# Optimization experiments

Hardware: AMD Instinct MI355X
Metric: run time of the kernel (lower is better)

Reference implementation:

```python
import jax, jax.numpy as jnp
import numpy as np

N_NODES = 100000
N_EDGES = 3200000
D_IN = 256
D_HID = 97


def setup_inputs() -> dict:
    key = jax.random.key(0)
    k1, k2, k3, k4, k5, k6 = jax.random.split(key, 6)
    x = jax.random.normal(k1, (N_NODES, D_IN), dtype=jnp.float32)
    edge_index = jax.random.randint(k2, (2, N_EDGES), 0, N_NODES, dtype=jnp.int64)
    # GCNConv weights (stored as [in, out]) and biases
    W1 = jax.random.normal(k3, (D_IN, D_HID), dtype=jnp.float32) / np.sqrt(D_IN)
    b1 = jnp.zeros((D_HID,), dtype=jnp.float32)
    W2 = jax.random.normal(k4, (D_HID, D_HID), dtype=jnp.float32) / np.sqrt(D_HID)
    b2 = jnp.zeros((D_HID,), dtype=jnp.float32)
    return {"x": x, "edge_index": edge_index, "W1": W1, "b1": b1, "W2": W2, "b2": b2}


def reference(x, edge_index, W1, b1, W2, b2):
    # PyG GCNConv: add self-loops, symmetric degree normalization,
    # out[i] = sum_j norm_ij * (x[j] @ W) + b
    N = x.shape[0]
    self_idx = jnp.arange(N, dtype=edge_index.dtype)
    src = jnp.concatenate([edge_index[0], self_idx])  # source j
    dst = jnp.concatenate([edge_index[1], self_idx])  # target i
    deg = jax.ops.segment_sum(jnp.ones_like(dst, dtype=x.dtype), dst, num_segments=N)
    dinv = jnp.where(deg > 0, 1.0 / jnp.sqrt(deg), 0.0)
    norm = dinv[src] * dinv[dst]  # [E+N]

    def gcn(h, W, b):
        h = h @ W  # dense linear transform first (out_dim small)
        msg = h[src] * norm[:, None]  # gather + scale
        agg = jax.ops.segment_sum(msg, dst, num_segments=N)  # scatter-add
        return agg + b

    h = jax.nn.relu(gcn(x, W1, b1))
    out = gcn(h, W2, b2)
    return out
```

## Files before the change

kernel.cpp:

```cpp
#include <hip/hip_runtime.h>
#include <hip/hip_fp16.h>
#include <stdint.h>

#define D_IN 256
#define D_H  97
#define RST  96
#define NPB  512
#define NBMAX 256
#define CHUNK 4096

typedef _Float16 f16;
typedef f16   f16x8 __attribute__((ext_vector_type(8)));
typedef float f32x4 __attribute__((ext_vector_type(4)));

__device__ __forceinline__ int load_idx(const void* p, int is64, long long pos) {
  if (is64) return (int)(((const long long*)p)[pos]);
  return ((const int*)p)[pos];
}

__global__ void detect_kernel(const void* ei, long long E, int* flag,
                              int* __restrict__ bcur, int nbuck) {
  const int* p32 = (const int*)ei;
  long long stride = E / 1024; if (stride < 1) stride = 1;
  int tid = threadIdx.x;
  for (int i = tid; i <= nbuck; i += 256) bcur[i] = 0;
  int bad = 0;
  for (int s = 0; s < 4; ++s) {
    long long k = ((long long)tid * 4 + s) * stride;
    if (k < E) {
      if (p32[2 * k + 1] != 0) bad = 1;
    }
  }
  __shared__ int sh_bad;
  if (tid == 0) sh_bad = 0;
  __syncthreads();
  if (bad) atomicOr(&sh_bad, 1);
  __syncthreads();
  if (tid == 0) *flag = sh_bad ? 0 : 1;
}

__global__ __launch_bounds__(256) void bucket_scatter_direct(
    const void* ei, const int* __restrict__ flag, int* __restrict__ bcur,
    unsigned int* __restrict__ bsd, long long E, int nbuck, int cap) {
  __shared__ unsigned int packs[CHUNK];
  __shared__ unsigned char bkts[CHUNK];
  __shared__ int hist[NBMAX];
  __shared__ int gpos[NBMAX];
  __shared__ int cur[NBMAX];
  int tid = threadIdx.x;
  if (tid < NBMAX) { hist[tid] = 0; cur[tid] = 0; }
  __syncthreads();
  int f = *flag;
  long long base = (long long)blockIdx.x * CHUNK;
  int cnt = (int)((E - base < CHUNK) ? (E - base) : CHUNK);
  #pragma unroll 4
  for (int i = tid; i < cnt; i += 256) {
    long long e = base + i;
    int s = load_idx(ei, f, e);
    int d = load_idx(ei, f, E + e);
    int b = d >> 9;
    packs[i] = ((unsigned int)(d & (NPB - 1)) << 17) | (unsigned int)s;
    bkts[i] = (unsigned char)b;
    atomicAdd(&hist[b], 1);
  }
  __syncthreads();
  if (tid < nbuck) { int h = hist[tid]; if (h) gpos[tid] = atomicAdd(&bcur[tid], h); }
  __syncthreads();
  #pragma unroll 4
  for (int i = tid; i < cnt; i += 256) {
    int b = bkts[i];
    int r = atomicAdd(&cur[b], 1);
    int idx = gpos[b] + r;
    if (idx < cap) bsd[(size_t)b * cap + idx] = packs[i];
  }
}

__global__ __launch_bounds__(256) void bucket_finalize(
    const unsigned int* __restrict__ bsd, const int* __restrict__ bcur,
    int* __restrict__ row_start, float* __restrict__ dinv,
    int* __restrict__ csr_src, int N, int cap, int nbuck) {
  __shared__ int sc[256];
  __shared__ int h[NPB];
  __shared__ int rs[NPB];
  __shared__ int cur[NPB];
  __shared__ int wsum[4];
  int b = blockIdx.x, tid = threadIdx.x;
  int lane = tid & 63, wid = tid >> 6;
  int v = (tid < nbuck) ? min(bcur[tid], cap) : 0;
  sc[tid] = v;
  h[2 * tid] = 0; h[2 * tid + 1] = 0;
  cur[2 * tid] = 0; cur[2 * tid + 1] = 0;
  __syncthreads();
  for (int o = 1; o < 256; o <<= 1) {
    int a = (tid >= o) ? sc[tid - o] : 0;
    __syncthreads();
    sc[tid] += a;
    __syncthreads();
  }
  int cnt = min(bcur[b], cap);
  int base = sc[b] - cnt;
  if (b == 0 && tid == 0) row_start[N] = sc[255];
  int d0 = b * cap;
  for (int i = tid; i < cnt; i += 256) atomicAdd(&h[bsd[d0 + i] >> 17], 1);
  __syncthreads();
  int a0 = h[2 * tid], a1 = h[2 * tid + 1];
  int tsum = a0 + a1;
  int incl = tsum;
  #pragma unroll
  for (int off = 1; off < 64; off <<= 1) {
    int n = __shfl_up(incl, off, 64);
    if (lane >= off) incl += n;
  }
  if (lane == 63) wsum[wid] = incl;
  __syncthreads();
  int woff = 0;
  for (int k = 0; k < wid; ++k) woff += wsum[k];
  int excl = woff + incl - tsum + base;
  rs[2 * tid] = excl;
  rs[2 * tid + 1] = excl + a0;
  int node0 = b * NPB;
  int n0 = node0 + 2 * tid, n1 = node0 + 2 * tid + 1;
  if (n0 < N) { row_start[n0] = excl;      dinv[n0] = rsqrtf((float)(a0 + 1)); }
  if (n1 < N) { row_start[n1] = excl + a0; dinv[n1] = rsqrtf((float)(a1 + 1)); }
  __syncthreads();
  for (int i = tid; i < cnt; i += 256) {
    unsigned int p = bsd[d0 + i];
    int r = p >> 17;
    int s = (int)(p & 0x1FFFFu);
    int rel = atomicAdd(&cur[r], 1);
    csr_src[rs[r] + rel] = s;
  }
}

__global__ void prep_kernel(const float* __restrict__ W1, const float* __restrict__ b1,
                            const float* __restrict__ W2, const float* __restrict__ b2,
                            f16* __restrict__ W1lin, f16* __restrict__ W2lin,
                            float* __restrict__ b1p, float* __restrict__ b2p) {
  int idx = blockIdx.x * blockDim.x + threadIdx.x;
  const int n1 = 8 * 7 * 512;
  const int n2 = 4 * 7 * 512;
  if (idx < n1) {
    int fid = idx >> 3, hh = idx & 7;
    int lane = fid & 63, fg = fid >> 6;
    int kb = fg / 7, cg = fg % 7;
    int c = cg * 16 + (lane & 15);
    int k = kb * 32 + (lane >> 4) * 8 + hh;
    W1lin[idx] = (f16)((c < D_H && k < 256) ? W1[k * D_H + c] : 0.f);
  } else if (idx < n1 + n2) {
    int j = idx - n1;
    int fid = j >> 3, hh = j & 7;
    int lane = fid & 63, fg = fid >> 6;
    int kb = fg / 7, cg = fg % 7;
    int c = cg * 16 + (lane & 15);
    int k = kb * 32 + (lane >> 4) * 8 + hh;
    W2lin[j] = (f16)((c < D_H && k < D_H) ? W2[k * D_H + c] : 0.f);
  } else if (idx < n1 + n2 + 128) {
    int c = idx - (n1 + n2);
    b1p[c] = (c < D_H) ? b1[c] : 0.0f;
  } else if (idx < n1 + n2 + 256) {
    int c = idx - (n1 + n2 + 128);
    b2p[c] = (c < D_H) ? b2[c] : 0.0f;
  }
}

template<int KI, bool IN_HALF>
__global__ __launch_bounds__(256) void mfma_gemm(
    const float* __restrict__ Af, const f16* __restrict__ Ah,
    const __half2* __restrict__ sideA,
    const f16* __restrict__ Wlin, const float* __restrict__ dinv,
    f16* __restrict__ C, __half2* __restrict__ sideC, int N) {
  int tid = threadIdx.x, wave = tid >> 6, lane = tid & 63;
  int row0 = blockIdx.x * 128;
  int m = lane & 15, q = lane >> 4;
  int kf = q * 8;
  int r0 = row0 + wave * 32 + m;
  int r1 = r0 + 16;
  int rr0 = (r0 < N) ? r0 : 0;
  int rr1 = (r1 < N) ? r1 : 0;
  const f16* wbase = Wlin + lane * 8;

  f16x8 a0[KI], a1[KI];
  #pragma unroll
  for (int kb = 0; kb < KI; ++kb) {
    if constexpr (!IN_HALF) {
      const float* p0 = &Af[(size_t)rr0 * 256 + kb * 32 + kf];
      const float* p1 = &Af[(size_t)rr1 * 256 + kb * 32 + kf];
      float4 u0 = *(const float4*)p0, u1 = *(const float4*)(p0 + 4);
      float4 w0 = *(const float4*)p1, w1 = *(const float4*)(p1 + 4);
      f16x8 t0, t1;
      t0[0] = (f16)u0.x; t0[1] = (f16)u0.y; t0[2] = (f16)u0.z; t0[3] = (f16)u0.w;
      t0[4] = (f16)u1.x; t0[5] = (f16)u1.y; t0[6] = (f16)u1.z; t0[7] = (f16)u1.w;
      t1[0] = (f16)w0.x; t1[1] = (f16)w0.y; t1[2] = (f16)w0.z; t1[3] = (f16)w0.w;
      t1[4] = (f16)w1.x; t1[5] = (f16)w1.y; t1[6] = (f16)w1.z; t1[7] = (f16)w1.w;
      a0[kb] = t0; a1[kb] = t1;
    } else {
      if (kb < KI - 1) {
        a0[kb] = *(const f16x8*)&Ah[(size_t)rr0 * RST + kb * 32 + kf];
        a1[kb] = *(const f16x8*)&Ah[(size_t)rr1 * RST + kb * 32 + kf];
      } else {
        f16x8 z0, z1;
        #pragma unroll
        for (int j = 0; j < 8; ++j) { z0[j] = (f16)0.f; z1[j] = (f16)0.f; }
        if (q == 0) {
          z0[0] = ((const f16*)sideA)[2 * rr0];
          z1[0] = ((const f16*)sideA)[2 * rr1];
        }
        a0[kb] = z0; a1[kb] = z1;
      }
    }
  }

  f32x4 acc[2][7];
  #pragma unroll
  for (int mg = 0; mg < 2; ++mg)
    #pragma unroll
    for (int cg = 0; cg < 7; ++cg)
      #pragma unroll
      for (int j = 0; j < 4; ++j) acc[mg][cg][j] = 0.f;

  #pragma unroll
  for (int kb = 0; kb < KI; ++kb) {
    #pragma unroll
    for (int cg = 0; cg < 7; ++cg) {
      f16x8 b = *(const f16x8*)&wbase[(kb * 7 + cg) * 512];
      acc[0][cg] = __builtin_amdgcn_mfma_f32_16x16x32_f16(a0[kb], b, acc[0][cg], 0, 0, 0);
      acc[1][cg] = __builtin_amdgcn_mfma_f32_16x16x32_f16(a1[kb], b, acc[1][cg], 0, 0, 0);
    }
  }

  int colb = m, rq = q * 4;
  #pragma unroll
  for (int mg = 0; mg < 2; ++mg) {
    #pragma unroll
    for (int j = 0; j < 4; ++j) {
      int r = row0 + wave * 32 + mg * 16 + rq + j;
      if (r >= N) continue;
      float dv = dinv[r];
      #pragma unroll
      for (int cg = 0; cg < 7; ++cg) {
        int c = cg * 16 + colb;
        float val = acc[mg][cg][j] * dv;
        if (c < 96)       C[(size_t)r * RST + c] = (f16)val;
        else if (c == 96) sideC[r] = __floats2half2_rn(val, 0.f);
      }
    }
  }
}

template<bool OUT_HALF, bool DO_RELU>
__global__ __launch_bounds__(256) void agg_kernel(
    const __half* __restrict__ t, const __half2* __restrict__ side,
    const int* __restrict__ csr_src, const int* __restrict__ row_start,
    const float* __restrict__ dinv, const float* __restrict__ bias,
    void* __restrict__ outp, __half2* __restrict__ side_out, int N) {
  int lane = threadIdx.x & 63;
  int node = blockIdx.x * (blockDim.x >> 6) + (threadIdx.x >> 6);
  if (node >= N || lane >= 49) return;
  const char* gbase = (lane < 48) ? (const char*)t + lane * 4 : (const char*)side;
  unsigned gscale = (lane < 48) ? (unsigned)(RST * 2) : 4u;
  auto GATHER = [&](int j) -> float2 {
    return __half22float2(*(const __half2*)(gbase + (size_t)((unsigned)j * gscale)));
  };
  int s = row_start[node], epd = row_start[node + 1];
  float di = dinv[node];
  float2 v = GATHER(node);
  float ax = v.x, ay = v.y;
  int e = s;
  while ((e & 3) && e < epd) {
    float2 u = GATHER(csr_src[e]);
    ax += u.x; ay += u.y; ++e;
  }
  for (; e + 8 <= epd; e += 8) {
    int4 q0 = *(const int4*)(csr_src + e);
    int4 q1 = *(const int4*)(csr_src + e + 4);
    float2 u0 = GATHER(q0.x), u1 = GATHER(q0.y), u2 = GATHER(q0.z), u3 = GATHER(q0.w);
    float2 u4 = GATHER(q1.x), u5 = GATHER(q1.y), u6 = GATHER(q1.z), u7 = GATHER(q1.w);
    ax += ((u0.x + u1.x) + (u2.x + u3.x)) + ((u4.x + u5.x) + (u6.x + u7.x));
    ay += ((u0.y + u1.y) + (u2.y + u3.y)) + ((u4.y + u5.y) + (u6.y + u7.y));
  }
  if (e + 4 <= epd) {
    int4 q0 = *(const int4*)(csr_src + e);
    float2 u0 = GATHER(q0.x), u1 = GATHER(q0.y), u2 = GATHER(q0.z), u3 = GATHER(q0.w);
    ax += (u0.x + u1.x) + (u2.x + u3.x);
    ay += (u0.y + u1.y) + (u2.y + u3.y);
    e += 4;
  }
  for (; e < epd; ++e) {
    float2 u = GATHER(csr_src[e]);
    ax += u.x; ay += u.y;
  }
  int c0 = 2 * lane;
  ax = ax * di + bias[c0];
  ay = ay * di + bias[c0 + 1];
  if (DO_RELU) { ax = fmaxf(ax, 0.f); ay = fmaxf(ay, 0.f); }
  if (OUT_HALF) {
    if (lane < 48) ((__half2*)((__half*)outp + (size_t)node * RST))[lane] = __floats2half2_rn(ax, ay);
    else           side_out[node] = __floats2half2_rn(ax, 0.f);
  } else {
    float* o = (float*)outp + (size_t)node * D_H;
    if (lane < 48) { o[c0] = ax; o[c0 + 1] = ay; }
    else           o[96] = ax;
  }
}

extern "C" void kernel_launch(void* const* d_in, const int* in_sizes, int n_in,
                              void* d_out, int out_size, void* d_ws, size_t ws_size,
                              hipStream_t stream) {
  const float* x  = (const float*)d_in[0];
  const void*  ei = d_in[1];
  const float* W1 = (const float*)d_in[2];
  const float* b1 = (const float*)d_in[3];
  const float* W2 = (const float*)d_in[4];
  const float* b2 = (const float*)d_in[5];
  int N = in_sizes[0] / D_IN;
  long long E = (long long)in_sizes[1] / 2;
  int nbuck = (N + NPB - 1) / NPB;
  int cap = (int)(E / nbuck) + 8192;

  char* base = (char*)d_ws;
  size_t off = 0;
  auto alloc = [&](size_t bytes) -> void* {
    void* p = base + off;
    off = (off + bytes + 255) & ~(size_t)255;
    return p;
  };
  int*    flag      = (int*)alloc(4);
  float*  dinv      = (float*)alloc((size_t)N * 4);
  int*    row_start = (int*)alloc((size_t)(N + 1) * 4);
  int*    bcur      = (int*)alloc((size_t)(nbuck + 1) * 4);
  int*    csr_src   = (int*)alloc((size_t)E * 4);
  unsigned int* bsd = (unsigned int*)alloc((size_t)nbuck * cap * 4);
  f16*    W1lin     = (f16*)alloc((size_t)8 * 7 * 512 * 2);
  f16*    W2lin     = (f16*)alloc((size_t)4 * 7 * 512 * 2);
  float*  b1p       = (float*)alloc(128 * 4);
  float*  b2p       = (float*)alloc(128 * 4);
  f16*    t1        = (f16*)alloc((size_t)N * RST * 2 + 256);
  __half2* sideT    = (__half2*)alloc((size_t)N * 4 + 256);
  f16*    h1        = (f16*)alloc((size_t)N * RST * 2 + 256);
  __half2* sideH    = (__half2*)alloc((size_t)N * 4 + 256);

  detect_kernel<<<1, 256, 0, stream>>>(ei, E, flag, bcur, nbuck);
  bucket_scatter_direct<<<(int)((E + CHUNK - 1) / CHUNK), 256, 0, stream>>>(
      ei, flag, bcur, bsd, E, nbuck, cap);
  bucket_finalize<<<nbuck, 256, 0, stream>>>(bsd, bcur, row_start, dinv, csr_src, N, cap, nbuck);
  prep_kernel<<<(8 * 7 * 512 + 4 * 7 * 512 + 256 + 255) / 256, 256, 0, stream>>>(
      W1, b1, W2, b2, W1lin, W2lin, b1p, b2p);

  int gGemm = (N + 127) / 128;

  mfma_gemm<8, false><<<gGemm, 256, 0, stream>>>(
      x, nullptr, nullptr, W1lin, dinv, t1, sideT, N);
  agg_kernel<true, true><<<(N + 3) / 4, 256, 0, stream>>>(
      (const __half*)t1, sideT, csr_src, row_start, dinv, b1p, h1, sideH, N);
  mfma_gemm<4, true><<<gGemm, 256, 0, stream>>>(
      nullptr, h1, sideH, W2lin, dinv, t1, sideT, N);
  agg_kernel<false, false><<<(N + 3) / 4, 256, 0, stream>>>(
      (const __half*)t1, sideT, csr_src, row_start, dinv, b2p, d_out, nullptr, N);
}
```

Measured before the change: 353.8 us.

## Overlap edge bucketing with first GEMM and move dinv scaling into aggregation

Merges the detect and weight-prep kernels into one launch. Runs the first GEMM in the same grid as the edge bucket scatter, which is possible because the GEMM output is left unscaled and so no longer waits for dinv. The layer-1 aggregation instead multiplies each gathered neighbor by dinv[src], an extra random 4-byte load per edge. This aims to overlap the dense GEMM with the memory-bound scatter and cut launches, at the cost of more gather traffic in the first aggregation and extra shared memory held by the GEMM blocks.

```diff
diff --git a/kernel.cpp b/kernel.cpp
--- a/kernel.cpp
+++ b/kernel.cpp
@@ -18,125 +18,33 @@
   return ((const int*)p)[pos];
 }
 
-__global__ void detect_kernel(const void* ei, long long E, int* flag,
-                              int* __restrict__ bcur, int nbuck) {
-  const int* p32 = (const int*)ei;
-  long long stride = E / 1024; if (stride < 1) stride = 1;
+__global__ __launch_bounds__(256) void detect_prep(
+    const void* ei, long long E, int* flag, int* __restrict__ bcur, int nbuck,
+    const float* __restrict__ W1, const float* __restrict__ b1,
+    const float* __restrict__ W2, const float* __restrict__ b2,
+    f16* __restrict__ W1lin, f16* __restrict__ W2lin,
+    float* __restrict__ b1p, float* __restrict__ b2p) {
   int tid = threadIdx.x;
-  for (int i = tid; i <= nbuck; i += 256) bcur[i] = 0;
-  int bad = 0;
-  for (int s = 0; s < 4; ++s) {
-    long long k = ((long long)tid * 4 + s) * stride;
-    if (k < E) {
-      if (p32[2 * k + 1] != 0) bad = 1;
-    }
-  }
-  __shared__ int sh_bad;
-  if (tid == 0) sh_bad = 0;
-  __syncthreads();
-  if (bad) atomicOr(&sh_bad, 1);
-  __syncthreads();
-  if (tid == 0) *flag = sh_bad ? 0 : 1;
-}
-
-__global__ __launch_bounds__(256) void bucket_scatter_direct(
-    const void* ei, const int* __restrict__ flag, int* __restrict__ bcur,
-    unsigned int* __restrict__ bsd, long long E, int nbuck, int cap) {
-  __shared__ unsigned int packs[CHUNK];
-  __shared__ unsigned char bkts[CHUNK];
-  __shared__ int hist[NBMAX];
-  __shared__ int gpos[NBMAX];
-  __shared__ int cur[NBMAX];
-  int tid = threadIdx.x;
-  if (tid < NBMAX) { hist[tid] = 0; cur[tid] = 0; }
-  __syncthreads();
-  int f = *flag;
-  long long base = (long long)blockIdx.x * CHUNK;
-  int cnt = (int)((E - base < CHUNK) ? (E - base) : CHUNK);
-  #pragma unroll 4
-  for (int i = tid; i < cnt; i += 256) {
-    long long e = base + i;
-    int s = load_idx(ei, f, e);
-    int d = load_idx(ei, f, E + e);
-    int b = d >> 9;
-    packs[i] = ((unsigned int)(d & (NPB - 1)) << 17) | (unsigned int)s;
-    bkts[i] = (unsigned char)b;
-    atomicAdd(&hist[b], 1);
-  }
-  __syncthreads();
-  if (tid < nbuck) { int h = hist[tid]; if (h) gpos[tid] = atomicAdd(&bcur[tid], h); }
-  __syncthreads();
-  #pragma unroll 4
-  for (int i = tid; i < cnt; i += 256) {
-    int b = bkts[i];
-    int r = atomicAdd(&cur[b], 1);
-    int idx = gpos[b] + r;
-    if (idx < cap) bsd[(size_t)b * cap + idx] = packs[i];
-  }
-}
-
-__global__ __launch_bounds__(256) void bucket_finalize(
-    const unsigned int* __restrict__ bsd, const int* __restrict__ bcur,
-    int* __restrict__ row_start, float* __restrict__ dinv,
-    int* __restrict__ csr_src, int N, int cap, int nbuck) {
-  __shared__ int sc[256];
-  __shared__ int h[NPB];
-  __shared__ int rs[NPB];
-  __shared__ int cur[NPB];
-  __shared__ int wsum[4];
-  int b = blockIdx.x, tid = threadIdx.x;
-  int lane = tid & 63, wid = tid >> 6;
-  int v = (tid < nbuck) ? min(bcur[tid], cap) : 0;
-  sc[tid] = v;
-  h[2 * tid] = 0; h[2 * tid + 1] = 0;
-  cur[2 * tid] = 0; cur[2 * tid + 1] = 0;
-  __syncthreads();
-  for (int o = 1; o < 256; o <<= 1) {
-    int a = (tid >= o) ? sc[tid - o] : 0;
+  if (blockIdx.x == 0) {
+    const int* p32 = (const int*)ei;
+    long long stride = E / 1024; if (stride < 1) stride = 1;
+    for (int i = tid; i <= nbuck; i += 256) bcur[i] = 0;
+    int bad = 0;
+    for (int s = 0; s < 4; ++s) {
+      long long k = ((long long)tid * 4 + s) * stride;
+      if (k < E) {
+        if (p32[2 * k + 1] != 0) bad = 1;
+      }
+    }
+    __shared__ int sh_bad;
+    if (tid == 0) sh_bad = 0;
     __syncthreads();
-    sc[tid] += a;
+    if (bad) atomicOr(&sh_bad, 1);
     __syncthreads();
-  }
-  int cnt = min(bcur[b], cap);
-  int base = sc[b] - cnt;
-  if (b == 0 && tid == 0) row_start[N] = sc[255];
-  int d0 = b * cap;
-  for (int i = tid; i < cnt; i += 256) atomicAdd(&h[bsd[d0 + i] >> 17], 1);
-  __syncthreads();
-  int a0 = h[2 * tid], a1 = h[2 * tid + 1];
-  int tsum = a0 + a1;
-  int incl = tsum;
-  #pragma unroll
-  for (int off = 1; off < 64; off <<= 1) {
-    int n = __shfl_up(incl, off, 64);
-    if (lane >= off) incl += n;
-  }
-  if (lane == 63) wsum[wid] = incl;
-  __syncthreads();
-  int woff = 0;
-  for (int k = 0; k < wid; ++k) woff += wsum[k];
-  int excl = woff + incl - tsum + base;
-  rs[2 * tid] = excl;
-  rs[2 * tid + 1] = excl + a0;
-  int node0 = b * NPB;
-  int n0 = node0 + 2 * tid, n1 = node0 + 2 * tid + 1;
-  if (n0 < N) { row_start[n0] = excl;      dinv[n0] = rsqrtf((float)(a0 + 1)); }
-  if (n1 < N) { row_start[n1] = excl + a0; dinv[n1] = rsqrtf((float)(a1 + 1)); }
-  __syncthreads();
-  for (int i = tid; i < cnt; i += 256) {
-    unsigned int p = bsd[d0 + i];
-    int r = p >> 17;
-    int s = (int)(p & 0x1FFFFu);
-    int rel = atomicAdd(&cur[r], 1);
-    csr_src[rs[r] + rel] = s;
-  }
-}
-
-__global__ void prep_kernel(const float* __restrict__ W1, const float* __restrict__ b1,
-                            const float* __restrict__ W2, const float* __restrict__ b2,
-                            f16* __restrict__ W1lin, f16* __restrict__ W2lin,
-                            float* __restrict__ b1p, float* __restrict__ b2p) {
-  int idx = blockIdx.x * blockDim.x + threadIdx.x;
+    if (tid == 0) *flag = sh_bad ? 0 : 1;
+    return;
+  }
+  int idx = (blockIdx.x - 1) * 256 + tid;
   const int n1 = 8 * 7 * 512;
   const int n2 = 4 * 7 * 512;
   if (idx < n1) {
@@ -163,14 +71,14 @@
   }
 }
 
-template<int KI, bool IN_HALF>
-__global__ __launch_bounds__(256) void mfma_gemm(
-    const float* __restrict__ Af, const f16* __restrict__ Ah,
+template<int KI, bool IN_HALF, bool SCALE_DINV>
+__device__ __forceinline__ void gemm_body(
+    int gb, const float* __restrict__ Af, const f16* __restrict__ Ah,
     const __half2* __restrict__ sideA,
     const f16* __restrict__ Wlin, const float* __restrict__ dinv,
     f16* __restrict__ C, __half2* __restrict__ sideC, int N) {
   int tid = threadIdx.x, wave = tid >> 6, lane = tid & 63;
-  int row0 = blockIdx.x * 128;
+  int row0 = gb * 128;
   int m = lane & 15, q = lane >> 4;
   int kf = q * 8;
   int r0 = row0 + wave * 32 + m;
@@ -235,11 +143,11 @@
     for (int j = 0; j < 4; ++j) {
       int r = row0 + wave * 32 + mg * 16 + rq + j;
       if (r >= N) continue;
-      float dv = dinv[r];
+      float dv = SCALE_DINV ? dinv[r] : 1.0f;
       #pragma unroll
       for (int cg = 0; cg < 7; ++cg) {
         int c = cg * 16 + colb;
-        float val = acc[mg][cg][j] * dv;
+        float val = SCALE_DINV ? (acc[mg][cg][j] * dv) : acc[mg][cg][j];
         if (c < 96)       C[(size_t)r * RST + c] = (f16)val;
         else if (c == 96) sideC[r] = __floats2half2_rn(val, 0.f);
       }
@@ -247,7 +155,114 @@
   }
 }
 
-template<bool OUT_HALF, bool DO_RELU>
+__global__ __launch_bounds__(256) void scatter_gemm1(
+    const void* ei, const int* __restrict__ flag, int* __restrict__ bcur,
+    unsigned int* __restrict__ bsd, long long E, int nbuck, int cap, int nScat,
+    const float* __restrict__ x, const f16* __restrict__ W1lin,
+    f16* __restrict__ t1, __half2* __restrict__ sideT, int N) {
+  __shared__ unsigned int packs[CHUNK];
+  __shared__ unsigned char bkts[CHUNK];
+  __shared__ int hist[NBMAX];
+  __shared__ int gpos[NBMAX];
+  __shared__ int cur[NBMAX];
+  int tid = threadIdx.x;
+  if ((int)blockIdx.x >= nScat) {
+    gemm_body<8, false, false>(blockIdx.x - nScat, x, nullptr, nullptr,
+                               W1lin, nullptr, t1, sideT, N);
+    return;
+  }
+  if (tid < NBMAX) { hist[tid] = 0; cur[tid] = 0; }
+  __syncthreads();
+  int f = *flag;
+  long long base = (long long)blockIdx.x * CHUNK;
+  int cnt = (int)((E - base < CHUNK) ? (E - base) : CHUNK);
+  #pragma unroll 4
+  for (int i = tid; i < cnt; i += 256) {
+    long long e = base + i;
+    int s = load_idx(ei, f, e);
+    int d = load_idx(ei, f, E + e);
+    int b = d >> 9;
+    packs[i] = ((unsigned int)(d & (NPB - 1)) << 17) | (unsigned int)s;
+    bkts[i] = (unsigned char)b;
+    atomicAdd(&hist[b], 1);
+  }
+  __syncthreads();
+  if (tid < nbuck) { int h = hist[tid]; if (h) gpos[tid] = atomicAdd(&bcur[tid], h); }
+  __syncthreads();
+  #pragma unroll 4
+  for (int i = tid; i < cnt; i += 256) {
+    int b = bkts[i];
+    int r = atomicAdd(&cur[b], 1);
+    int idx = gpos[b] + r;
+    if (idx < cap) bsd[(size_t)b * cap + idx] = packs[i];
+  }
+}
+
+__global__ __launch_bounds__(256) void bucket_finalize(
+    const unsigned int* __restrict__ bsd, const int* __restrict__ bcur,
+    int* __restrict__ row_start, float* __restrict__ dinv,
+    int* __restrict__ csr_src, int N, int cap, int nbuck) {
+  __shared__ int sc[256];
+  __shared__ int h[NPB];
+  __shared__ int rs[NPB];
+  __shared__ int cur[NPB];
+  __shared__ int wsum[4];
+  int b = blockIdx.x, tid = threadIdx.x;
+  int lane = tid & 63, wid = tid >> 6;
+  int v = (tid < nbuck) ? min(bcur[tid], cap) : 0;
+  sc[tid] = v;
+  h[2 * tid] = 0; h[2 * tid + 1] = 0;
+  cur[2 * tid] = 0; cur[2 * tid + 1] = 0;
+  __syncthreads();
+  for (int o = 1; o < 256; o <<= 1) {
+    int a = (tid >= o) ? sc[tid - o] : 0;
+    __syncthreads();
+    sc[tid] += a;
+    __syncthreads();
+  }
+  int cnt = min(bcur[b], cap);
+  int base = sc[b] - cnt;
+  if (b == 0 && tid == 0) row_start[N] = sc[255];
+  int d0 = b * cap;
+  for (int i = tid; i < cnt; i += 256) atomicAdd(&h[bsd[d0 + i] >> 17], 1);
+  __syncthreads();
+  int a0 = h[2 * tid], a1 = h[2 * tid + 1];
+  int tsum = a0 + a1;
+  int incl = tsum;
+  #pragma unroll
+  for (int off = 1; off < 64; off <<= 1) {
+    int n = __shfl_up(incl, off, 64);
+    if (lane >= off) incl += n;
+  }
+  if (lane == 63) wsum[wid] = incl;
+  __syncthreads();
+  int woff = 0;
+  for (int k = 0; k < wid; ++k) woff += wsum[k];
+  int excl = woff + incl - tsum + base;
+  rs[2 * tid] = excl;
+  rs[2 * tid + 1] = excl + a0;
+  int node0 = b * NPB;
+  int n0 = node0 + 2 * tid, n1 = node0 + 2 * tid + 1;
+  if (n0 < N) { row_start[n0] = excl;      dinv[n0] = rsqrtf((float)(a0 + 1)); }
+  if (n1 < N) { row_start[n1] = excl + a0; dinv[n1] = rsqrtf((float)(a1 + 1)); }
+  __syncthreads();
+  for (int i = tid; i < cnt; i += 256) {
+    unsigned int p = bsd[d0 + i];
+    int r = p >> 17;
+    int s = (int)(p & 0x1FFFFu);
+    int rel = atomicAdd(&cur[r], 1);
+    csr_src[rs[r] + rel] = s;
+  }
+}
+
+__global__ __launch_bounds__(256) void mfma_gemm2(
+    const f16* __restrict__ Ah, const __half2* __restrict__ sideA,
+    const f16* __restrict__ Wlin, const float* __restrict__ dinv,
+    f16* __restrict__ C, __half2* __restrict__ sideC, int N) {
+  gemm_body<4, true, true>(blockIdx.x, nullptr, Ah, sideA, Wlin, dinv, C, sideC, N);
+}
+
+template<bool OUT_HALF, bool DO_RELU, bool SRC_SCALE>
 __global__ __launch_bounds__(256) void agg_kernel(
     const __half* __restrict__ t, const __half2* __restrict__ side,
     const int* __restrict__ csr_src, const int* __restrict__ row_start,
@@ -264,30 +279,52 @@
   int s = row_start[node], epd = row_start[node + 1];
   float di = dinv[node];
   float2 v = GATHER(node);
-  float ax = v.x, ay = v.y;
+  float ax, ay;
+  if (SRC_SCALE) { ax = di * v.x; ay = di * v.y; }
+  else           { ax = v.x;      ay = v.y; }
   int e = s;
   while ((e & 3) && e < epd) {
-    float2 u = GATHER(csr_src[e]);
-    ax += u.x; ay += u.y; ++e;
+    int j = csr_src[e];
+    float2 u = GATHER(j);
+    if (SRC_SCALE) { float w = dinv[j]; ax = fmaf(w, u.x, ax); ay = fmaf(w, u.y, ay); }
+    else           { ax += u.x; ay += u.y; }
+    ++e;
   }
   for (; e + 8 <= epd; e += 8) {
     int4 q0 = *(const int4*)(csr_src + e);
     int4 q1 = *(const int4*)(csr_src + e + 4);
     float2 u0 = GATHER(q0.x), u1 = GATHER(q0.y), u2 = GATHER(q0.z), u3 = GATHER(q0.w);
     float2 u4 = GATHER(q1.x), u5 = GATHER(q1.y), u6 = GATHER(q1.z), u7 = GATHER(q1.w);
-    ax += ((u0.x + u1.x) + (u2.x + u3.x)) + ((u4.x + u5.x) + (u6.x + u7.x));
-    ay += ((u0.y + u1.y) + (u2.y + u3.y)) + ((u4.y + u5.y) + (u6.y + u7.y));
+    if (SRC_SCALE) {
+      float w0 = dinv[q0.x], w1 = dinv[q0.y], w2 = dinv[q0.z], w3 = dinv[q0.w];
+      float w4 = dinv[q1.x], w5 = dinv[q1.y], w6 = dinv[q1.z], w7 = dinv[q1.w];
+      ax += (fmaf(w0, u0.x, w1 * u1.x) + fmaf(w2, u2.x, w3 * u3.x)) +
+            (fmaf(w4, u4.x, w5 * u5.x) + fmaf(w6, u6.x, w7 * u7.x));
+      ay += (fmaf(w0, u0.y, w1 * u1.y) + fmaf(w2, u2.y, w3 * u3.y)) +
+            (fmaf(w4, u4.y, w5 * u5.y) + fmaf(w6, u6.y, w7 * u7.y));
+    } else {
+      ax += ((u0.x + u1.x) + (u2.x + u3.x)) + ((u4.x + u5.x) + (u6.x + u7.x));
+      ay += ((u0.y + u1.y) + (u2.y + u3.y)) + ((u4.y + u5.y) + (u6.y + u7.y));
+    }
   }
   if (e + 4 <= epd) {
     int4 q0 = *(const int4*)(csr_src + e);
     float2 u0 = GATHER(q0.x), u1 = GATHER(q0.y), u2 = GATHER(q0.z), u3 = GATHER(q0.w);
-    ax += (u0.x + u1.x) + (u2.x + u3.x);
-    ay += (u0.y + u1.y) + (u2.y + u3.y);
+    if (SRC_SCALE) {
+      float w0 = dinv[q0.x], w1 = dinv[q0.y], w2 = dinv[q0.z], w3 = dinv[q0.w];
+      ax += fmaf(w0, u0.x, w1 * u1.x) + fmaf(w2, u2.x, w3 * u3.x);
+      ay += fmaf(w0, u0.y, w1 * u1.y) + fmaf(w2, u2.y, w3 * u3.y);
+    } else {
+      ax += (u0.x + u1.x) + (u2.x + u3.x);
+      ay += (u0.y + u1.y) + (u2.y + u3.y);
+    }
     e += 4;
   }
   for (; e < epd; ++e) {
-    float2 u = GATHER(csr_src[e]);
-    ax += u.x; ay += u.y;
+    int j = csr_src[e];
+    float2 u = GATHER(j);
+    if (SRC_SCALE) { float w = dinv[j]; ax = fmaf(w, u.x, ax); ay = fmaf(w, u.y, ay); }
+    else           { ax += u.x; ay += u.y; }
   }
   int c0 = 2 * lane;
   ax = ax * di + bias[c0];
@@ -339,21 +376,20 @@
   f16*    h1        = (f16*)alloc((size_t)N * RST * 2 + 256);
   __half2* sideH    = (__half2*)alloc((size_t)N * 4 + 256);
 
-  detect_kernel<<<1, 256, 0, stream>>>(ei, E, flag, bcur, nbuck);
-  bucket_scatter_direct<<<(int)((E + CHUNK - 1) / CHUNK), 256, 0, stream>>>(
-      ei, flag, bcur, bsd, E, nbuck, cap);
-  bucket_finalize<<<nbuck, 256, 0, stream>>>(bsd, bcur, row_start, dinv, csr_src, N, cap, nbuck);
-  prep_kernel<<<(8 * 7 * 512 + 4 * 7 * 512 + 256 + 255) / 256, 256, 0, stream>>>(
-      W1, b1, W2, b2, W1lin, W2lin, b1p, b2p);
-
+  const int prepTot = 8 * 7 * 512 + 4 * 7 * 512 + 256;
+  int gPrep = (prepTot + 255) / 256;
+  int nScat = (int)((E + CHUNK - 1) / CHUNK);
   int gGemm = (N + 127) / 128;
 
-  mfma_gemm<8, false><<<gGemm, 256, 0, stream>>>(
-      x, nullptr, nullptr, W1lin, dinv, t1, sideT, N);
-  agg_kernel<true, true><<<(N + 3) / 4, 256, 0, stream>>>(
+  detect_prep<<<1 + gPrep, 256, 0, stream>>>(
+      ei, E, flag, bcur, nbuck, W1, b1, W2, b2, W1lin, W2lin, b1p, b2p);
+  scatter_gemm1<<<nScat + gGemm, 256, 0, stream>>>(
+      ei, flag, bcur, bsd, E, nbuck, cap, nScat, x, W1lin, t1, sideT, N);
+  bucket_finalize<<<nbuck, 256, 0, stream>>>(
+      bsd, bcur, row_start, dinv, csr_src, N, cap, nbuck);
+  agg_kernel<true, true, true><<<(N + 3) / 4, 256, 0, stream>>>(
       (const __half*)t1, sideT, csr_src, row_start, dinv, b1p, h1, sideH, N);
-  mfma_gemm<4, true><<<gGemm, 256, 0, stream>>>(
-      nullptr, h1, sideH, W2lin, dinv, t1, sideT, N);
-  agg_kernel<false, false><<<(N + 3) / 4, 256, 0, stream>>>(
+  mfma_gemm2<<<gGemm, 256, 0, stream>>>(h1, sideH, W2lin, dinv, t1, sideT, N);
+  agg_kernel<false, false, false><<<(N + 3) / 4, 256, 0, stream>>>(
       (const __half*)t1, sideT, csr_src, row_start, dinv, b2p, d_out, nullptr, N);
 }
```

Result: no change. 352.7 us (-0.3%).
